# Kernel tuning notes

Measured on AMD Instinct MI355X. Metric: run time of the kernel, lower is better.

## Reference

```python
import jax, jax.numpy as jnp
import numpy as np
import math

D = 2048
NH = 16
DH = D // NH
LAT = D // 4
B, S = 2, 2048
EPS = 1e-5


def _ln(x, g, b):
    m = jnp.mean(x, axis=-1, keepdims=True)
    v = jnp.mean((x - m) ** 2, axis=-1, keepdims=True)
    return (x - m) * jax.lax.rsqrt(v + EPS) * g + b


def setup_inputs() -> dict:
    key = jax.random.key(0)
    ks = jax.random.split(key, 12)
    p = lambda k, shape: 0.01 * jax.random.normal(k, shape, dtype=jnp.float32)
    return {
        "x": jax.random.normal(ks[0], (B, S, D), dtype=jnp.float32),
        "W_dq": p(ks[1], (D, LAT)),
        "W_uq": p(ks[2], (LAT, D)),
        "q_ln_g": jnp.ones((LAT,), jnp.float32),
        "q_ln_b": jnp.zeros((LAT,), jnp.float32),
        "W_dkv": p(ks[3], (D, LAT)),
        "W_ukv": p(ks[4], (LAT, 2 * D)),
        "kv_ln_g": jnp.ones((LAT,), jnp.float32),
        "kv_ln_b": jnp.zeros((LAT,), jnp.float32),
        "W_o": p(ks[5], (D, D)),
        "norm1_g": jnp.ones((D,), jnp.float32),
        "norm1_b": jnp.zeros((D,), jnp.float32),
        "norm2_g": jnp.ones((D,), jnp.float32),
        "norm2_b": jnp.zeros((D,), jnp.float32),
        "fc1_w": p(ks[6], (4 * D, D)),
        "fc1_b": jnp.zeros((4 * D,), jnp.float32),
        "fc2_w": p(ks[7], (D, 4 * D)),
        "fc2_b": jnp.zeros((D,), jnp.float32),
    }


def reference(x, W_dq, W_uq, q_ln_g, q_ln_b, W_dkv, W_ukv, kv_ln_g, kv_ln_b,
              W_o, norm1_g, norm1_b, norm2_g, norm2_b, fc1_w, fc1_b, fc2_w, fc2_b):
    normed = _ln(x, norm1_g, norm1_b)

    # --- RopelessMLA attention ---
    cq = _ln(normed @ W_dq, q_ln_g, q_ln_b)          # [B,S,LAT]
    Q = cq @ W_uq                                     # [B,S,D]
    ckv = _ln(normed @ W_dkv, kv_ln_g, kv_ln_b)       # [B,S,LAT]
    KV = ckv @ W_ukv                                  # [B,S,2D]
    K, V = KV[..., :D], KV[..., D:]

    q = Q.reshape(B, S, NH, DH)
    k = K.reshape(B, S, NH, DH)
    v = V.reshape(B, S, NH, DH)

    qkt = jnp.einsum("bqhd,bkhd->bhqk", q, k) / math.sqrt(float(DH))
    mask = jnp.tril(jnp.ones((S, S), dtype=qkt.dtype))  # causal, past_length=0
    qkt = qkt * mask
    qkt = jnp.where(qkt == 0.0, -jnp.inf, qkt)  # faithful to original zero->-inf trick
    attn = jax.nn.softmax(qkt, axis=-1)
    o = jnp.einsum("bhqk,bkhd->bqhd", attn, v).reshape(B, S, D)
    mh_x = o @ W_o.T

    x = x + mh_x
    h = _ln(x, norm2_g, norm2_b)
    h = jax.nn.relu(h @ fc1_w.T + fc1_b)
    h = h @ fc2_w.T + fc2_b  # dropout is identity in eval mode
    return x + h
```

## Files before the change

### kernel.cpp

```cpp
#include <hip/hip_runtime.h>
#include <hip/hip_bf16.h>


#define DEVI __device__ __forceinline__

typedef __attribute__((ext_vector_type(8))) short bf16x8;
typedef __attribute__((ext_vector_type(4))) float f32x4;

DEVI unsigned short f2bf(float f) {
  union { float f; unsigned u; } v; v.f = f;
  unsigned r = v.u + 0x7fffu + ((v.u >> 16) & 1u);
  return (unsigned short)(r >> 16);
}

DEVI float bf2f(unsigned short u) {
  union { unsigned u; float f; } v; v.u = ((unsigned)u) << 16;
  return v.f;
}

#define GLDS16(gp, lp)                                              \
  __builtin_amdgcn_global_load_lds(                                 \
      (__attribute__((address_space(1))) void*)(gp),                \
      (__attribute__((address_space(3))) void*)(lp), 16, 0, 0)

#define NEG_INF (-__builtin_inff())

DEVI float blockReduceSum(float v) {
  v += __shfl_xor(v, 1);  v += __shfl_xor(v, 2);  v += __shfl_xor(v, 4);
  v += __shfl_xor(v, 8);  v += __shfl_xor(v, 16); v += __shfl_xor(v, 32);
  __shared__ float red[4];
  if ((threadIdx.x & 63) == 0) red[threadIdx.x >> 6] = v;
  __syncthreads();
  v = red[0] + red[1] + red[2] + red[3];
  __syncthreads();
  return v;
}

__global__ __launch_bounds__(256) void cast2_f32_bf16(
    const float* __restrict__ in1, unsigned short* __restrict__ out1, long n1,
    const float* __restrict__ in2, unsigned short* __restrict__ out2) {
  long i = ((long)blockIdx.x * 256 + threadIdx.x) * 4;
  const float* in = in1;
  unsigned short* out = out1;
  if (i >= n1) { i -= n1; in = in2; out = out2; }
  const float4 v = *reinterpret_cast<const float4*>(in + i);
  ushort4 o;
  o.x = f2bf(v.x); o.y = f2bf(v.y); o.z = f2bf(v.z); o.w = f2bf(v.w);
  *reinterpret_cast<ushort4*>(out + i) = o;
}

__global__ __launch_bounds__(256) void weight_prep(
    const float* __restrict__ W_dq, const float* __restrict__ W_dkv,
    const float* __restrict__ W_uq, const float* __restrict__ W_ukv,
    const float* __restrict__ W_o, unsigned short* __restrict__ dqkv_t,
    unsigned short* __restrict__ uq_t, unsigned short* __restrict__ ukv_t,
    unsigned short* __restrict__ wo_b,
    const float* __restrict__ x, const float* __restrict__ n1g,
    const float* __restrict__ n1b, unsigned short* __restrict__ normed) {
  __shared__ float tile[32][33];
  const int id = blockIdx.x;
  const int tx = threadIdx.x & 31, ty = threadIdx.x >> 5;
  const float* in;
  unsigned short* out;
  int R, C, bx, by;
  if (id < 1024) {
    in = W_dq; out = dqkv_t; R = 2048; C = 512; bx = id & 15; by = id >> 4;
  } else if (id < 2048) {
    const int t = id - 1024;
    in = W_dkv; out = dqkv_t + 512 * 2048; R = 2048; C = 512; bx = t & 15; by = t >> 4;
  } else if (id < 3072) {
    const int t = id - 2048;
    in = W_uq; out = uq_t; R = 512; C = 2048; bx = t & 63; by = t >> 6;
  } else if (id < 5120) {
    const int t = id - 3072;
    in = W_ukv; out = ukv_t; R = 512; C = 4096; bx = t & 127; by = t >> 7;
  } else if (id < 9216) {
    const long i = ((long)(id - 5120) * 256 + threadIdx.x) * 4;
    const float4 v = *reinterpret_cast<const float4*>(W_o + i);
    ushort4 o;
    o.x = f2bf(v.x); o.y = f2bf(v.y); o.z = f2bf(v.z); o.w = f2bf(v.w);
    *reinterpret_cast<ushort4*>(wo_b + i) = o;
    return;
  } else {
    const long row = id - 9216;
    const float* xr = x + row * 2048;
    float v[8];
    float s = 0.f;
#pragma unroll
    for (int i = 0; i < 8; i++) { v[i] = xr[threadIdx.x + i * 256]; s += v[i]; }
    s = blockReduceSum(s);
    const float mean = s * (1.0f / 2048.f);
    float s2 = 0.f;
#pragma unroll
    for (int i = 0; i < 8; i++) { float d = v[i] - mean; s2 += d * d; }
    s2 = blockReduceSum(s2);
    const float rstd = rsqrtf(s2 * (1.0f / 2048.f) + 1e-5f);
#pragma unroll
    for (int i = 0; i < 8; i++) {
      const int c = threadIdx.x + i * 256;
      normed[row * 2048 + c] = f2bf((v[i] - mean) * rstd * n1g[c] + n1b[c]);
    }
    return;
  }
  const int c0 = bx * 32, r0 = by * 32;
#pragma unroll
  for (int i = 0; i < 32; i += 8)
    tile[ty + i][tx] = in[(long)(r0 + ty + i) * C + c0 + tx];
  __syncthreads();
#pragma unroll
  for (int i = 0; i < 32; i += 8)
    out[(long)(c0 + ty + i) * R + r0 + tx] = f2bf(tile[tx][ty + i]);
}

__global__ __launch_bounds__(256) void ln2x512(
    const unsigned short* __restrict__ part, const float* __restrict__ g1,
    const float* __restrict__ b1, const float* __restrict__ g2,
    const float* __restrict__ b2, unsigned short* __restrict__ cq,
    unsigned short* __restrict__ ckv) {
  constexpr long PN = 4096L * 1024;
  const long row = blockIdx.x;
  const int tid = threadIdx.x;
  const int half = tid >> 7, lt = tid & 127;
  __shared__ float red[8];
  const long off = row * 1024 + half * 512 + lt * 4;
  const ushort4 a0 = *reinterpret_cast<const ushort4*>(part + off);
  const ushort4 a1 = *reinterpret_cast<const ushort4*>(part + PN + off);
  const ushort4 a2 = *reinterpret_cast<const ushort4*>(part + 2 * PN + off);
  const ushort4 a3 = *reinterpret_cast<const ushort4*>(part + 3 * PN + off);
  float4 v;
  v.x = bf2f(a0.x) + bf2f(a1.x) + bf2f(a2.x) + bf2f(a3.x);
  v.y = bf2f(a0.y) + bf2f(a1.y) + bf2f(a2.y) + bf2f(a3.y);
  v.z = bf2f(a0.z) + bf2f(a1.z) + bf2f(a2.z) + bf2f(a3.z);
  v.w = bf2f(a0.w) + bf2f(a1.w) + bf2f(a2.w) + bf2f(a3.w);
  float s = v.x + v.y + v.z + v.w;
  s += __shfl_xor(s, 1);  s += __shfl_xor(s, 2);  s += __shfl_xor(s, 4);
  s += __shfl_xor(s, 8);  s += __shfl_xor(s, 16); s += __shfl_xor(s, 32);
  if ((tid & 63) == 0) red[tid >> 6] = s;
  __syncthreads();
  const float mean = (red[half * 2] + red[half * 2 + 1]) * (1.f / 512.f);
  const float d0 = v.x - mean, d1 = v.y - mean, d2 = v.z - mean, d3 = v.w - mean;
  float s2 = d0 * d0 + d1 * d1 + d2 * d2 + d3 * d3;
  s2 += __shfl_xor(s2, 1);  s2 += __shfl_xor(s2, 2);  s2 += __shfl_xor(s2, 4);
  s2 += __shfl_xor(s2, 8);  s2 += __shfl_xor(s2, 16); s2 += __shfl_xor(s2, 32);
  if ((tid & 63) == 0) red[4 + (tid >> 6)] = s2;
  __syncthreads();
  const float rstd = rsqrtf((red[4 + half * 2] + red[5 + half * 2]) * (1.f / 512.f) + 1e-5f);
  const float* g = half ? g2 : g1;
  const float* b = half ? b2 : b1;
  const float4 gv = *reinterpret_cast<const float4*>(g + lt * 4);
  const float4 bv = *reinterpret_cast<const float4*>(b + lt * 4);
  ushort4 o;
  o.x = f2bf(d0 * rstd * gv.x + bv.x);
  o.y = f2bf(d1 * rstd * gv.y + bv.y);
  o.z = f2bf(d2 * rstd * gv.z + bv.z);
  o.w = f2bf(d3 * rstd * gv.w + bv.w);
  *reinterpret_cast<ushort4*>((half ? ckv : cq) + row * 512 + lt * 4) = o;
}

__global__ __launch_bounds__(256) void combine_ln(
    const unsigned short* __restrict__ p, const float* __restrict__ xres,
    const float* __restrict__ g, const float* __restrict__ b,
    float* __restrict__ x2, unsigned short* __restrict__ h1, long n) {
  const int c0 = threadIdx.x * 8;
  const long base = (long)blockIdx.x * 2048 + c0;
  float v[8];
  float s = 0.f;
#pragma unroll
  for (int hh = 0; hh < 2; hh++) {
    const long i = base + hh * 4;
    const ushort4 a  = *reinterpret_cast<const ushort4*>(p + i);
    const ushort4 bb = *reinterpret_cast<const ushort4*>(p + n + i);
    const float4 r = *reinterpret_cast<const float4*>(xres + i);
    float4 o;
    o.x = r.x + bf2f(a.x) + bf2f(bb.x);
    o.y = r.y + bf2f(a.y) + bf2f(bb.y);
    o.z = r.z + bf2f(a.z) + bf2f(bb.z);
    o.w = r.w + bf2f(a.w) + bf2f(bb.w);
    *reinterpret_cast<float4*>(x2 + i) = o;
    v[hh * 4 + 0] = o.x; v[hh * 4 + 1] = o.y;
    v[hh * 4 + 2] = o.z; v[hh * 4 + 3] = o.w;
    s += o.x + o.y + o.z + o.w;
  }
  s = blockReduceSum(s);
  const float mean = s * (1.0f / 2048.f);
  float s2 = 0.f;
#pragma unroll
  for (int i = 0; i < 8; i++) { float d = v[i] - mean; s2 += d * d; }
  s2 = blockReduceSum(s2);
  const float rstd = rsqrtf(s2 * (1.0f / 2048.f) + 1e-5f);
#pragma unroll
  for (int hh = 0; hh < 2; hh++) {
    const float4 gv = *reinterpret_cast<const float4*>(g + c0 + hh * 4);
    const float4 bv = *reinterpret_cast<const float4*>(b + c0 + hh * 4);
    ushort4 o;
    o.x = f2bf((v[hh * 4 + 0] - mean) * rstd * gv.x + bv.x);
    o.y = f2bf((v[hh * 4 + 1] - mean) * rstd * gv.y + bv.y);
    o.z = f2bf((v[hh * 4 + 2] - mean) * rstd * gv.z + bv.z);
    o.w = f2bf((v[hh * 4 + 3] - mean) * rstd * gv.w + bv.w);
    *reinterpret_cast<ushort4*>(h1 + base + hh * 4) = o;
  }
}

template <bool BIAS, bool RELU, bool OBF16, bool VT, bool MIX>
__global__ __launch_bounds__(512, 1) void gemm256p(
    const unsigned short* __restrict__ A, const unsigned short* __restrict__ Bt,
    const float* __restrict__ bias, void* __restrict__ Cout,
    unsigned short* __restrict__ VtOut,
    const unsigned short* __restrict__ A2, const unsigned short* __restrict__ Bt2,
    void* __restrict__ Cout2,
    int M, int N, int lda, int ldb, int kLen, long kOff) {
  __shared__ __align__(16) unsigned short L[2][2][2][256 * 32];

  const int m0 = blockIdx.x * 256;
  int n0 = blockIdx.y * 256;
  int Nn = N;
  const unsigned short* Ap = A;
  const unsigned short* Btp = Bt;
  void* Coutp = Cout;
  bool isQ = false;
  if (MIX && blockIdx.y >= 16) {
    isQ = true;
    Ap = A2; Btp = Bt2; Coutp = Cout2;
    n0 = (blockIdx.y - 16) * 256;
    Nn = 2048;
  }
  const long ka = (long)blockIdx.z * kOff;
  const int tid = threadIdx.x;
  const int lane = tid & 63, w = tid >> 6;
  const int sr = (w >> 2) * 64, sc = (w & 3) * 32;
  const int g = lane >> 4, lrow = lane & 15;
  const int r_ = tid >> 2, s_ = tid & 3;

  f32x4 acc[2][2][4][2] = {};
  const int nt = kLen >> 6;

#define STG1(bb, ab, h, kh, t, P, base0, ld)                                   \
  {                                                                            \
    const long k0 = ka + (long)(t) * 64 + (kh) * 32;                           \
    const int rr = (h) * 128 + r_;                                             \
    GLDS16((P) + (long)((base0) + rr) * (ld) + k0 + ((s_ ^ ((rr >> 1) & 3)) << 3), \
           &L[bb][ab][kh][((h) * 512 + tid) * 8]);                             \
  }
#define STG_A(bb, h, t) STG1(bb, 0, h, 0, t, Ap, m0, lda) STG1(bb, 0, h, 1, t, Ap, m0, lda)
#define STG_B(bb, h, t) STG1(bb, 1, h, 0, t, Btp, n0, ldb) STG1(bb, 1, h, 1, t, Btp, n0, ldb)

#define RD_A(fa, bu, a)                                                        \
  _Pragma("unroll")                                                            \
  for (int kh = 0; kh < 2; kh++)                                               \
    _Pragma("unroll")                                                          \
    for (int i = 0; i < 4; i++) {                                              \
      const int rr = (a) * 128 + sr + i * 16 + lrow;                           \
      fa[kh][i] = *reinterpret_cast<const bf16x8*>(                            \
          &L[bu][0][kh][(rr * 4 + (g ^ ((rr >> 1) & 3))) * 8]);                \
    }
#define RD_B(fb, bu, b)                                                        \
  _Pragma("unroll")                                                            \
  for (int kh = 0; kh < 2; kh++)                                               \
    _Pragma("unroll")                                                          \
    for (int j = 0; j < 2; j++) {                                              \
      const int rr = (b) * 128 + sc + j * 16 + lrow;                           \
      fb[kh][j] = *reinterpret_cast<const bf16x8*>(                            \
          &L[bu][1][kh][(rr * 4 + (g ^ ((rr >> 1) & 3))) * 8]);                \
    }

#define PH_MFMA(a, b)                                                          \
  __builtin_amdgcn_s_setprio(1);                                               \
  _Pragma("unroll")                                                            \
  for (int kh = 0; kh < 2; kh++)                                               \
    _Pragma("unroll")                                                          \
    for (int i = 0; i < 4; i++)                                                \
      _Pragma("unroll")                                                        \
      for (int j = 0; j < 2; j++)                                              \
        acc[a][b][i][j] = __builtin_amdgcn_mfma_f32_16x16x32_bf16(             \
            fa[kh][i], fb[kh][j], acc[a][b][i][j], 0, 0, 0);                   \
  __builtin_amdgcn_s_setprio(0);

  STG_A(0, 0, 0) STG_B(0, 0, 0) STG_B(0, 1, 0) STG_A(0, 1, 0)
  asm volatile("s_waitcnt vmcnt(0)\n\ts_barrier" ::: "memory");

  for (int t = 0; t < nt; t++) {
    const int bu = t & 1, bn = bu ^ 1;
    const bool pf = (t + 1 < nt);
    bf16x8 fa[2][4], fb[2][2];
    RD_A(fa, bu, 0)
    RD_B(fb, bu, 0)
    if (pf) STG_A(bn, 0, t + 1)
    PH_MFMA(0, 0)
    RD_B(fb, bu, 1)
    if (pf) STG_B(bn, 1, t + 1)
    PH_MFMA(0, 1)
    if (pf) asm volatile("s_waitcnt vmcnt(4)\n\ts_barrier" ::: "memory");
    else    asm volatile("s_waitcnt vmcnt(0)\n\ts_barrier" ::: "memory");
    RD_A(fa, bu, 1)
    if (pf) STG_B(bn, 0, t + 1)
    PH_MFMA(1, 1)
    RD_B(fb, bu, 0)
    if (pf) STG_A(bn, 1, t + 1)
    PH_MFMA(1, 0)
    if (pf) asm volatile("s_waitcnt vmcnt(2)\n\ts_barrier" ::: "memory");
  }
#undef STG1
#undef STG_A
#undef STG_B
#undef RD_A
#undef RD_B
#undef PH_MFMA

  const long zoff = (long)blockIdx.z * (long)M * (long)Nn;
  if (VT && !isQ && n0 >= 2048) {
#pragma unroll
    for (int a = 0; a < 2; a++) {
#pragma unroll
      for (int b = 0; b < 2; b++) {
#pragma unroll
        for (int i = 0; i < 4; i++) {
#pragma unroll
          for (int j = 0; j < 2; j++) {
            const int row0 = m0 + a * 128 + sr + i * 16 + g * 4;
            const int col2 = n0 + b * 128 + sc + j * 16 + lrow - 2048;
            const int hh = col2 >> 7, dd = col2 & 127;
            const int batch = row0 >> 11, sseq = row0 & 2047;
            ushort4 o;
            o.x = f2bf(acc[a][b][i][j][0]);
            o.y = f2bf(acc[a][b][i][j][1]);
            o.z = f2bf(acc[a][b][i][j][2]);
            o.w = f2bf(acc[a][b][i][j][3]);
            *reinterpret_cast<ushort4*>(
                VtOut + ((long)((batch * 16 + hh) * 128 + dd)) * 2048 + sseq) = o;
          }
        }
      }
    }
    return;
  }
#pragma unroll
  for (int a = 0; a < 2; a++) {
#pragma unroll
    for (int b = 0; b < 2; b++) {
#pragma unroll
      for (int i = 0; i < 4; i++) {
#pragma unroll
        for (int j = 0; j < 2; j++) {
          const int row = m0 + a * 128 + sr + i * 16 + g * 4;
          const int col = n0 + b * 128 + sc + j * 16 + lrow;
          float bv = 0.f;
          if (BIAS) bv = bias[col];
#pragma unroll
          for (int r = 0; r < 4; r++) {
            float v = acc[a][b][i][j][r];
            if (BIAS) v += bv;
            if (RELU) v = fmaxf(v, 0.f);
            const long idx = zoff + (long)(row + r) * Nn + col;
            if (OBF16) ((unsigned short*)Coutp)[idx] = f2bf(v);
            else       ((float*)Coutp)[idx] = v;
          }
        }
      }
    }
  }
}

template <bool BIAS>
__global__ __launch_bounds__(256) void combine2(
    const unsigned short* __restrict__ p, const float* __restrict__ bias,
    const float* __restrict__ res, float* __restrict__ out, long n) {
  const long i = ((long)blockIdx.x * 256 + threadIdx.x) * 4;
  if (i >= n) return;
  const ushort4 a = *reinterpret_cast<const ushort4*>(p + i);
  const ushort4 b = *reinterpret_cast<const ushort4*>(p + n + i);
  const float4 r = *reinterpret_cast<const float4*>(res + i);
  float4 o;
  o.x = bf2f(a.x) + bf2f(b.x) + r.x;
  o.y = bf2f(a.y) + bf2f(b.y) + r.y;
  o.z = bf2f(a.z) + bf2f(b.z) + r.z;
  o.w = bf2f(a.w) + bf2f(b.w) + r.w;
  if (BIAS) {
    const int col = (int)(i & 2047);
    const float4 bv = *reinterpret_cast<const float4*>(bias + col);
    o.x += bv.x; o.y += bv.y; o.z += bv.z; o.w += bv.w;
  }
  *reinterpret_cast<float4*>(out + i) = o;
}

__global__ __launch_bounds__(256) void flash_attn(
    const unsigned short* __restrict__ Q, const unsigned short* __restrict__ KV,
    const unsigned short* __restrict__ Vt, unsigned short* __restrict__ O) {
  constexpr int S = 2048;
  const int tid = threadIdx.x, lane = tid & 63, w = tid >> 6;
  const int g = lane >> 4, lcol = lane & 15;
  const int wg = blockIdx.x;
  const int x8 = wg & 7, q64 = wg >> 3;
  const int p = q64 & 15, hi = q64 >> 4;
  const int bh = x8 * 4 + hi;
  const int b = bh >> 4, h = bh & 15;
  const long kvrow0 = (long)b * S;
  const int hd0 = h * 128;

  __shared__ __align__(16) unsigned short Kl[64 * 128];
  __shared__ __align__(16) unsigned short Vl[128 * 64];
  __shared__ __align__(16) unsigned short Pl[4 * 16 * 64];

  const float kscale = 0.08838834764831845f * 1.4426950408889634f;

  for (int ti = 0; ti < 2; ti++) {
    const int t = ti ? (31 - p) : p;
    const int qbase = t * 64;
    bf16x8 qf[4];
#pragma unroll
    for (int dc = 0; dc < 4; dc++)
      qf[dc] = *reinterpret_cast<const bf16x8*>(
          Q + (kvrow0 + qbase + w * 16 + lcol) * 2048 + hd0 + dc * 32 + g * 8);
    f32x4 oacc[8] = {};
    float mst[4] = {NEG_INF, NEG_INF, NEG_INF, NEG_INF};
    float lst[4] = {0.f, 0.f, 0.f, 0.f};
    const int nk = t + 1;
    for (int kt = 0; kt < nk; kt++) {
      const int kv0 = kt * 64;
      __syncthreads();
#pragma unroll
      for (int i = 0; i < 4; i++) {
        const int o16 = i * 256 + tid;
        const int kr = o16 >> 4, ks = o16 & 15;
        GLDS16(KV + (kvrow0 + kv0 + kr) * 4096 + hd0 + 8 * (ks ^ (kr & 7)),
               Kl + o16 * 8);
        const int vd = o16 >> 3, vs = o16 & 7;
        GLDS16(Vt + ((long)bh * 128 + vd) * 2048 + kv0 + 8 * (vs ^ (vd & 7)),
               Vl + o16 * 8);
      }
      __syncthreads();
      f32x4 sc[4] = {};
      __builtin_amdgcn_s_setprio(1);
#pragma unroll
      for (int dc = 0; dc < 4; dc++) {
#pragma unroll
        for (int c = 0; c < 4; c++) {
          const bf16x8 kf = *reinterpret_cast<const bf16x8*>(
              Kl + (c * 16 + lcol) * 128 + 8 * ((4 * dc + g) ^ (lcol & 7)));
          sc[c] = __builtin_amdgcn_mfma_f32_16x16x32_bf16(qf[dc], kf, sc[c], 0, 0, 0);
        }
      }
      __builtin_amdgcn_s_setprio(0);
      float s[4][4];
      const int qrow = qbase + w * 16 + g * 4;
      if (kt == nk - 1) {
#pragma unroll
        for (int c = 0; c < 4; c++) {
          const int col = kv0 + c * 16 + lcol;
#pragma unroll
          for (int r = 0; r < 4; r++)
            s[c][r] = (col <= qrow + r) ? sc[c][r] * kscale : NEG_INF;
        }
      } else {
#pragma unroll
        for (int c = 0; c < 4; c++)
#pragma unroll
          for (int r = 0; r < 4; r++) s[c][r] = sc[c][r] * kscale;
      }
      float pm[4];
#pragma unroll
      for (int r = 0; r < 4; r++) {
        float mx = fmaxf(fmaxf(s[0][r], s[1][r]), fmaxf(s[2][r], s[3][r]));
        mx = fmaxf(mx, __shfl_xor(mx, 1));
        mx = fmaxf(mx, __shfl_xor(mx, 2));
        mx = fmaxf(mx, __shfl_xor(mx, 4));
        mx = fmaxf(mx, __shfl_xor(mx, 8));
        pm[r] = mx;
      }
      bool need = false;
#pragma unroll
      for (int r = 0; r < 4; r++) need = need || (pm[r] > mst[r] + 11.5f);
      if (__any(need)) {
#pragma unroll
        for (int r = 0; r < 4; r++) {
          const float mnew = fmaxf(mst[r], pm[r]);
          const float corr = exp2f(mst[r] - mnew);
          mst[r] = mnew;
          lst[r] *= corr;
#pragma unroll
          for (int db = 0; db < 8; db++) oacc[db][r] *= corr;
        }
      }
#pragma unroll
      for (int r = 0; r < 4; r++) {
        float ps = 0.f;
#pragma unroll
        for (int c = 0; c < 4; c++) {
          const float pv = exp2f(s[c][r] - mst[r]);
          Pl[(w * 16 + g * 4 + r) * 64 + c * 16 + lcol] = f2bf(pv);
          ps += pv;
        }
        ps += __shfl_xor(ps, 1); ps += __shfl_xor(ps, 2);
        ps += __shfl_xor(ps, 4); ps += __shfl_xor(ps, 8);
        lst[r] += ps;
      }
      __builtin_amdgcn_s_setprio(1);
#pragma unroll
      for (int kk = 0; kk < 2; kk++) {
        const bf16x8 pf = *reinterpret_cast<const bf16x8*>(
            Pl + (w * 16 + lcol) * 64 + kk * 32 + g * 8);
#pragma unroll
        for (int db = 0; db < 8; db++) {
          const bf16x8 vf = *reinterpret_cast<const bf16x8*>(
              Vl + (db * 16 + lcol) * 64 + 8 * ((4 * kk + g) ^ (lcol & 7)));
          oacc[db] = __builtin_amdgcn_mfma_f32_16x16x32_bf16(pf, vf, oacc[db], 0, 0, 0);
        }
      }
      __builtin_amdgcn_s_setprio(0);
    }
#pragma unroll
    for (int db = 0; db < 8; db++)
#pragma unroll
      for (int r = 0; r < 4; r++) {
        const int qi = qbase + w * 16 + g * 4 + r;
        O[(kvrow0 + qi) * 2048 + hd0 + db * 16 + lcol] = f2bf(oacc[db][r] / lst[r]);
      }
  }
}

extern "C" void kernel_launch(void* const* d_in, const int* in_sizes, int n_in,
                              void* d_out, int out_size, void* d_ws, size_t ws_size,
                              hipStream_t stream) {
  (void)in_sizes; (void)n_in; (void)out_size; (void)ws_size;
  const float* x     = (const float*)d_in[0];
  const float* W_dq  = (const float*)d_in[1];
  const float* W_uq  = (const float*)d_in[2];
  const float* qlng  = (const float*)d_in[3];
  const float* qlnb  = (const float*)d_in[4];
  const float* W_dkv = (const float*)d_in[5];
  const float* W_ukv = (const float*)d_in[6];
  const float* klng  = (const float*)d_in[7];
  const float* klnb  = (const float*)d_in[8];
  const float* W_o   = (const float*)d_in[9];
  const float* n1g   = (const float*)d_in[10];
  const float* n1b   = (const float*)d_in[11];
  const float* n2g   = (const float*)d_in[12];
  const float* n2b   = (const float*)d_in[13];
  const float* fc1w  = (const float*)d_in[14];
  const float* fc1b  = (const float*)d_in[15];
  const float* fc2w  = (const float*)d_in[16];
  const float* fc2b  = (const float*)d_in[17];
  float* out = (float*)d_out;

  char* ws = (char*)d_ws;
  unsigned short* normed = (unsigned short*)(ws + 0);
  unsigned short* Obuf   = (unsigned short*)(ws + 0);
  unsigned short* fc2bb  = (unsigned short*)(ws + 0);
  unsigned short* cqkv_part = (unsigned short*)(ws + 33554432);
  unsigned short* KV        = (unsigned short*)(ws + 33554432);
  unsigned short* fc1bb     = (unsigned short*)(ws + 33554432);
  unsigned short* fc2part   = (unsigned short*)(ws + 33554432);
  unsigned short* cq  = (unsigned short*)(ws + 67108864);
  unsigned short* Qb = (unsigned short*)(ws + 71303168);
  unsigned short* h1 = (unsigned short*)(ws + 71303168);
  unsigned short* ckv = (unsigned short*)(ws + 88080384);
  float* x2           = (float*)(ws + 88080384);
  unsigned short* Vtb    = (unsigned short*)(ws + 121634816);
  unsigned short* wopart = (unsigned short*)(ws + 121634816);
  unsigned short* hmid   = (unsigned short*)(ws + 121634816);
  unsigned short* dqkv_t = (unsigned short*)(ws + 188743680);
  unsigned short* uq_t   = dqkv_t + 2097152;
  unsigned short* ukv_t  = uq_t + 1048576;
  unsigned short* wo_b   = ukv_t + 2097152;

  const dim3 blk(256);
  const dim3 blk8(512);

  weight_prep<<<13312, blk, 0, stream>>>(W_dq, W_dkv, W_uq, W_ukv, W_o,
                                         dqkv_t, uq_t, ukv_t, wo_b,
                                         x, n1g, n1b, normed);

  gemm256p<false, false, true, false, false><<<dim3(16, 4, 4), blk8, 0, stream>>>(
      normed, dqkv_t, nullptr, cqkv_part, nullptr, nullptr, nullptr, nullptr,
      4096, 1024, 2048, 2048, 512, 512);
  ln2x512<<<4096, blk, 0, stream>>>(cqkv_part, qlng, qlnb, klng, klnb, cq, ckv);
  gemm256p<false, false, true, true, true><<<dim3(16, 24), blk8, 0, stream>>>(
      ckv, ukv_t, nullptr, KV, Vtb, cq, uq_t, Qb,
      4096, 4096, 512, 512, 512, 0);
  flash_attn<<<dim3(512), blk, 0, stream>>>(Qb, KV, Vtb, Obuf);
  gemm256p<false, false, true, false, false><<<dim3(16, 8, 2), blk8, 0, stream>>>(
      Obuf, wo_b, nullptr, wopart, nullptr, nullptr, nullptr, nullptr,
      4096, 2048, 2048, 2048, 1024, 1024);
  cast2_f32_bf16<<<32768, blk, 0, stream>>>(fc1w, fc1bb, 16777216L, fc2w, fc2bb);
  combine_ln<<<4096, blk, 0, stream>>>(wopart, x, n2g, n2b, x2, h1, 8388608L);
  gemm256p<true, true, true, false, false><<<dim3(16, 32), blk8, 0, stream>>>(
      h1, fc1bb, fc1b, hmid, nullptr, nullptr, nullptr, nullptr,
      4096, 8192, 2048, 2048, 2048, 0);
  gemm256p<false, false, true, false, false><<<dim3(16, 8, 2), blk8, 0, stream>>>(
      hmid, fc2bb, nullptr, fc2part, nullptr, nullptr, nullptr, nullptr,
      4096, 2048, 8192, 8192, 4096, 4096);
  combine2<true><<<8192, blk, 0, stream>>>(fc2part, fc2b, x2, out, 8388608L);
}
```

Baseline: 520.3 us.

## Split flash attention KV loop across two workgroups and merge partials

Result: slower. 533.7 us (+2.6%).

```diff
diff --git a/kernel.cpp b/kernel.cpp
--- a/kernel.cpp
+++ b/kernel.cpp
@@ -384,17 +384,23 @@
 
 __global__ __launch_bounds__(256) void flash_attn(
     const unsigned short* __restrict__ Q, const unsigned short* __restrict__ KV,
-    const unsigned short* __restrict__ Vt, unsigned short* __restrict__ O) {
+    const unsigned short* __restrict__ Vt, unsigned short* __restrict__ O0,
+    unsigned short* __restrict__ O1, float* __restrict__ ML) {
   constexpr int S = 2048;
   const int tid = threadIdx.x, lane = tid & 63, w = tid >> 6;
   const int g = lane >> 4, lcol = lane & 15;
   const int wg = blockIdx.x;
-  const int x8 = wg & 7, q64 = wg >> 3;
+  const int x8 = wg & 7;
+  const int rest = wg >> 3;
+  const int hf = rest & 1;
+  const int q64 = rest >> 1;
   const int p = q64 & 15, hi = q64 >> 4;
   const int bh = x8 * 4 + hi;
   const int b = bh >> 4, h = bh & 15;
   const long kvrow0 = (long)b * S;
   const int hd0 = h * 128;
+  unsigned short* Op = hf ? O1 : O0;
+  float* mlp = ML + hf * 131072;
 
   __shared__ __align__(16) unsigned short Kl[64 * 128];
   __shared__ __align__(16) unsigned short Vl[128 * 64];
@@ -414,7 +420,7 @@
     float mst[4] = {NEG_INF, NEG_INF, NEG_INF, NEG_INF};
     float lst[4] = {0.f, 0.f, 0.f, 0.f};
     const int nk = t + 1;
-    for (int kt = 0; kt < nk; kt++) {
+    for (int kt = hf; kt < nk; kt += 2) {
       const int kv0 = kt * 64;
       __syncthreads();
 #pragma unroll
@@ -442,7 +448,7 @@
       __builtin_amdgcn_s_setprio(0);
       float s[4][4];
       const int qrow = qbase + w * 16 + g * 4;
-      if (kt == nk - 1) {
+      if (kt == t) {
 #pragma unroll
         for (int c = 0; c < 4; c++) {
           const int col = kv0 + c * 16 + lcol;
@@ -512,9 +518,51 @@
 #pragma unroll
       for (int r = 0; r < 4; r++) {
         const int qi = qbase + w * 16 + g * 4 + r;
-        O[(kvrow0 + qi) * 2048 + hd0 + db * 16 + lcol] = f2bf(oacc[db][r] / lst[r]);
-      }
-  }
+        Op[(kvrow0 + qi) * 2048 + hd0 + db * 16 + lcol] = f2bf(oacc[db][r]);
+      }
+    if (lcol == 0) {
+#pragma unroll
+      for (int r = 0; r < 4; r++) {
+        const int qi = qbase + w * 16 + g * 4 + r;
+        mlp[(bh * 2048 + qi) * 2] = mst[r];
+        mlp[(bh * 2048 + qi) * 2 + 1] = lst[r];
+      }
+    }
+  }
+}
+
+__global__ __launch_bounds__(256) void merge_attn(
+    const unsigned short* __restrict__ P0, const unsigned short* __restrict__ P1,
+    const float* __restrict__ ML, unsigned short* __restrict__ O) {
+  const int tid = threadIdx.x;
+  const int rh = blockIdx.x * 16 + (tid >> 4);
+  const int d0 = (tid & 15) * 8;
+  const int bs = rh >> 4;
+  const int h = rh & 15;
+  const int b = bs >> 11, qi = bs & 2047;
+  const int bh = b * 16 + h;
+  const int mlidx = (bh * 2048 + qi) * 2;
+  const float m0 = ML[mlidx], l0 = ML[mlidx + 1];
+  const float m1 = ML[131072 + mlidx], l1 = ML[131072 + mlidx + 1];
+  const float m = fmaxf(m0, m1);
+  const float w0 = exp2f(m0 - m), w1 = exp2f(m1 - m);
+  const float dn = 1.f / (w0 * l0 + w1 * l1);
+  const long off = (long)bs * 2048 + h * 128 + d0;
+  const ushort4 a0 = *reinterpret_cast<const ushort4*>(P0 + off);
+  const ushort4 a1 = *reinterpret_cast<const ushort4*>(P0 + off + 4);
+  const ushort4 c0 = *reinterpret_cast<const ushort4*>(P1 + off);
+  const ushort4 c1 = *reinterpret_cast<const ushort4*>(P1 + off + 4);
+  ushort4 o0, o1;
+  o0.x = f2bf((w0 * bf2f(a0.x) + w1 * bf2f(c0.x)) * dn);
+  o0.y = f2bf((w0 * bf2f(a0.y) + w1 * bf2f(c0.y)) * dn);
+  o0.z = f2bf((w0 * bf2f(a0.z) + w1 * bf2f(c0.z)) * dn);
+  o0.w = f2bf((w0 * bf2f(a0.w) + w1 * bf2f(c0.w)) * dn);
+  o1.x = f2bf((w0 * bf2f(a1.x) + w1 * bf2f(c1.x)) * dn);
+  o1.y = f2bf((w0 * bf2f(a1.y) + w1 * bf2f(c1.y)) * dn);
+  o1.z = f2bf((w0 * bf2f(a1.z) + w1 * bf2f(c1.z)) * dn);
+  o1.w = f2bf((w0 * bf2f(a1.w) + w1 * bf2f(c1.w)) * dn);
+  *reinterpret_cast<ushort4*>(O + off) = o0;
+  *reinterpret_cast<ushort4*>(O + off + 4) = o1;
 }
 
 extern "C" void kernel_launch(void* const* d_in, const int* in_sizes, int n_in,
@@ -543,18 +591,21 @@
 
   char* ws = (char*)d_ws;
   unsigned short* normed = (unsigned short*)(ws + 0);
-  unsigned short* Obuf   = (unsigned short*)(ws + 0);
+  unsigned short* Op0    = (unsigned short*)(ws + 0);
   unsigned short* fc2bb  = (unsigned short*)(ws + 0);
   unsigned short* cqkv_part = (unsigned short*)(ws + 33554432);
   unsigned short* KV        = (unsigned short*)(ws + 33554432);
+  unsigned short* Obuf      = (unsigned short*)(ws + 33554432);
   unsigned short* fc1bb     = (unsigned short*)(ws + 33554432);
   unsigned short* fc2part   = (unsigned short*)(ws + 33554432);
   unsigned short* cq  = (unsigned short*)(ws + 67108864);
   unsigned short* Qb = (unsigned short*)(ws + 71303168);
   unsigned short* h1 = (unsigned short*)(ws + 71303168);
   unsigned short* ckv = (unsigned short*)(ws + 88080384);
+  unsigned short* Op1 = (unsigned short*)(ws + 88080384);
   float* x2           = (float*)(ws + 88080384);
   unsigned short* Vtb    = (unsigned short*)(ws + 121634816);
+  float* MLbuf           = (float*)(ws + 138412032);
   unsigned short* wopart = (unsigned short*)(ws + 121634816);
   unsigned short* hmid   = (unsigned short*)(ws + 121634816);
   unsigned short* dqkv_t = (unsigned short*)(ws + 188743680);
@@ -576,7 +627,8 @@
   gemm256p<false, false, true, true, true><<<dim3(16, 24), blk8, 0, stream>>>(
       ckv, ukv_t, nullptr, KV, Vtb, cq, uq_t, Qb,
       4096, 4096, 512, 512, 512, 0);
-  flash_attn<<<dim3(512), blk, 0, stream>>>(Qb, KV, Vtb, Obuf);
+  flash_attn<<<dim3(1024), blk, 0, stream>>>(Qb, KV, Vtb, Op0, Op1, MLbuf);
+  merge_attn<<<4096, blk, 0, stream>>>(Op0, Op1, MLbuf, Obuf);
   gemm256p<false, false, true, false, false><<<dim3(16, 8, 2), blk8, 0, stream>>>(
       Obuf, wo_b, nullptr, wopart, nullptr, nullptr, nullptr, nullptr,
       4096, 2048, 2048, 2048, 1024, 1024);
```
